# Kernel optimization log

Hardware: AMD Instinct MI355X
Metric: run time of the kernel (lower is better)

## Reference

```python
import jax, jax.numpy as jnp
import numpy as np


def lstm_cell(x, h, c, Wi, Wh, b):
    # PyTorch LSTMCell gate order: i, f, g, o
    g = x @ Wi.T + h @ Wh.T + b
    i, f, gg, o = jnp.split(g, 4, axis=-1)
    c = jax.nn.sigmoid(f) * c + jax.nn.sigmoid(i) * jnp.tanh(gg)
    h = jax.nn.sigmoid(o) * jnp.tanh(c)
    return h, c


def setup_inputs() -> dict:
    key = jax.random.key(0)
    ks = jax.random.split(key, 32)
    S, B, L, N, T = 20, 16, 30, 6, 20
    H, E, Vs, Vt = 512, 512, 50000, 30000
    w = lambda k, shape: jax.random.normal(k, shape, jnp.float32) * 0.05
    return {
        'articles': jax.random.randint(ks[0], (S, B, L), 0, Vs, jnp.int32),
        'summaries': jax.random.randint(ks[1], (N, B, T), 0, Vt, jnp.int32),
        'emb_src': w(ks[2], (Vs, E)),
        'emb_tgt': w(ks[3], (Vt, E)),
        'we_Wi': w(ks[4], (4 * H, E)), 'we_Wh': w(ks[5], (4 * H, H)), 'we_b': w(ks[6], (4 * H,)),
        'se_Wi': w(ks[7], (4 * H, H)), 'se_Wh': w(ks[8], (4 * H, H)), 'se_b': w(ks[9], (4 * H,)),
        'W_feat': w(ks[10], (H, H)), 'b_feat': w(ks[11], (H,)),
        'wd_Wi': w(ks[12], (4 * H, E)), 'wd_Wh': w(ks[13], (4 * H, H)), 'wd_b': w(ks[14], (4 * H,)),
        'W_vocab': w(ks[15], (Vt, H)), 'b_vocab': w(ks[16], (Vt,)),
        'sd_Wi': w(ks[17], (4 * H, H)), 'sd_Wh': w(ks[18], (4 * H, H)), 'sd_b': w(ks[19], (4 * H,)),
        'attn_Wh': w(ks[20], (H, H)), 'attn_wc': w(ks[21], (H,)), 'attn_v': w(ks[22], (H,)),
        'W_out': w(ks[23], (H, 2 * H)), 'b_out': w(ks[24], (H,)),
    }


def _forward(articles, summaries, emb_src, emb_tgt, we_Wi, we_Wh, we_b,
             se_Wi, se_Wh, se_b, W_feat, b_feat, wd_Wi, wd_Wh, wd_b,
             W_vocab, b_vocab, sd_Wi, sd_Wh, sd_b, attn_Wh, attn_wc, attn_v,
             W_out, b_out):
    S, B, L = articles.shape
    H = we_Wh.shape[1]

    # ---- word encoder: LSTMCell over each sentence, vmapped over S ----
    def encode_sentence(tokens):  # [B, L]
        x = emb_src[tokens]  # [B, L, E]
        z = jnp.zeros((B, H), x.dtype)
        def step(hc, xt):
            h, c = lstm_cell(xt, hc[0], hc[1], we_Wi, we_Wh, we_b)
            return (h, c), None
        (h, _), _ = jax.lax.scan(step, (z, z), jnp.swapaxes(x, 0, 1))
        return h
    word_hx = jax.vmap(encode_sentence)(articles)  # [S, B, H]

    # ---- sentence encoder: LSTM over sentence dim ----
    z = jnp.zeros((B, H), word_hx.dtype)
    def senc_step(hc, x):
        h, c = lstm_cell(x, hc[0], hc[1], se_Wi, se_Wh, se_b)
        return (h, c), h
    (s_hx, s_cx), sent_out = jax.lax.scan(senc_step, (z, z), word_hx)  # sent_out [S,B,H]
    sent_feat = sent_out @ W_feat.T + b_feat  # precomputed attention features

    mask = (articles[:, :, 0:1] > 0).astype(jnp.float32)  # [S, B, 1]
    coverage0 = jnp.zeros_like(mask)

    # ---- hierarchical decoder over summary sentences ----
    def sent_step(carry, sent):  # sent [B, T]
        w_hx, w_cx, s_hx, s_cx, coverage, loss = carry
        seq = sent.T  # [T, B]

        def word_step(wc, ba):
            wh, wcell, l = wc
            wb, wa = ba
            wh, wcell = lstm_cell(emb_tgt[wb], wh, wcell, wd_Wi, wd_Wh, wd_b)
            logits = wh @ W_vocab.T + b_vocab  # [B, V]
            logp = jax.nn.log_softmax(logits, axis=-1)
            nll = -jnp.take_along_axis(logp, wa[:, None], axis=1)[:, 0]
            m = (wa != 0).astype(logits.dtype)  # ignore_index=0
            l = l + jnp.sum(nll * m) / jnp.maximum(jnp.sum(m), 1.0)
            return (wh, wcell, l), None

        (w_hx, w_cx, loss), _ = jax.lax.scan(word_step, (w_hx, w_cx, loss), (seq[:-1], seq[1:]))

        # sentence decoder step with coverage attention over S sentences
        s_h2, s_cx = lstm_cell(w_hx, s_hx, s_cx, sd_Wi, sd_Wh, sd_b)
        e = jnp.einsum('sbh,h->sb', jnp.tanh(sent_feat + s_h2 @ attn_Wh.T + coverage * attn_wc), attn_v)
        e = jnp.where(mask[:, :, 0] > 0, e, -1e9)
        align = jax.nn.softmax(e, axis=0)[:, :, None]  # [S, B, 1]
        context = jnp.sum(align * sent_out, axis=0)  # [B, H]
        final = jnp.tanh(jnp.concatenate([context, s_h2], axis=-1) @ W_out.T + b_out)
        # coverage loss (with pre-update coverage), then accumulate coverage
        loss = loss + jnp.mean(jnp.sum(jnp.minimum(align[:, :, 0], coverage[:, :, 0]), axis=0))
        coverage = coverage + align
        return (final, w_cx, final, s_cx, coverage, loss), None

    init = (s_hx, s_cx, s_hx, s_cx, coverage0, jnp.float32(0.0))
    (_, _, _, _, _, loss), _ = jax.lax.scan(sent_step, init, summaries)
    return loss


def reference(articles, summaries, emb_src, emb_tgt, we_Wi, we_Wh, we_b,
              se_Wi, se_Wh, se_b, W_feat, b_feat, wd_Wi, wd_Wh, wd_b,
              W_vocab, b_vocab, sd_Wi, sd_Wh, sd_b, attn_Wh, attn_wc, attn_v,
              W_out, b_out):
    return _forward(articles, summaries, emb_src, emb_tgt, we_Wi, we_Wh, we_b,
                    se_Wi, se_Wh, se_b, W_feat, b_feat, wd_Wi, wd_Wh, wd_b,
                    W_vocab, b_vocab, sd_Wi, sd_Wh, sd_b, attn_Wh, attn_wc,
                    attn_v, W_out, b_out)
```

## Files before the change

### kernel.cpp

```cpp
#include <hip/hip_runtime.h>
#include <cstdint>
#include <cstddef>

#define H 512
#define SS 20
#define BB 16
#define LL 30
#define NN 6
#define TT 20
#define VT 30000
#define MROWS 1824
#define NSTEPS 114
#define MPAD 1856
#define NT2 120
#define UBLK 16
#define NV 232
#define MEGA 248

#define SCOPE_AGENT __HIP_MEMORY_SCOPE_AGENT

typedef __attribute__((ext_vector_type(8))) short bf16x8;
typedef __attribute__((ext_vector_type(4))) float f32x4;

__device__ __forceinline__ float sigmoidf_(float x) { return 1.f / (1.f + expf(-x)); }
__device__ __forceinline__ float b2f(ushort u) { return __uint_as_float(((uint32_t)u) << 16); }
__device__ __forceinline__ ushort f2b_rne(float f) {
  uint32_t u = __float_as_uint(f);
  return (ushort)((u + 0x7fffu + ((u >> 16) & 1u)) >> 16);
}

__device__ __forceinline__ void ast_u32(uint* p, uint v) {
  __hip_atomic_store(p, v, __ATOMIC_RELAXED, SCOPE_AGENT);
}
__device__ __forceinline__ uint ald_u32(const uint* p) {
  return __hip_atomic_load(p, __ATOMIC_RELAXED, SCOPE_AGENT);
}

__device__ __forceinline__ void sbar(uint* flags, int slot, int nblk, uint phase)
{
  __syncthreads();
  if (threadIdx.x == 0) {
    __builtin_amdgcn_fence(__ATOMIC_RELEASE, "agent");
    ast_u32(&flags[slot * 16], phase);
  }
  if ((int)threadIdx.x < nblk) {
    while (ald_u32(&flags[threadIdx.x * 16]) < phase)
      __builtin_amdgcn_s_sleep(1);
  }
  __syncthreads();
  if (threadIdx.x == 0)
    __builtin_amdgcn_fence(__ATOMIC_ACQUIRE, "agent");
  __syncthreads();
}

struct PrepP {
  const int* articles; const int* summaries;
  const float* emb_src; const float* emb_tgt;
  const float* we_Wi; const float* wd_Wi; const float* we_Wh;
  const float* se_Wi; const float* se_Wh; const float* W_feat;
  const float* wd_Wh; const float* sd_Wi; const float* sd_Wh;
  const float* attn_Wh; const float* W_out;
  ushort* A_we; ushort* A_wd;
  ushort* weWi; ushort* wdWi; ushort* weWh;
  ushort* seWi; ushort* seWh; ushort* wfeat;
  ushort* wdWh; ushort* sdWi; ushort* sdWh;
  ushort* attnWh; ushort* Wout;
};

__device__ __forceinline__ void conv_f2b(const float* __restrict__ src,
                                         ushort* __restrict__ dst, int n4,
                                         int t0, int stride)
{
  for (int i = t0; i < n4; i += stride) {
    float4 v = reinterpret_cast<const float4*>(src)[i];
    ushort4 o;
    o.x = f2b_rne(v.x); o.y = f2b_rne(v.y);
    o.z = f2b_rne(v.z); o.w = f2b_rne(v.w);
    reinterpret_cast<ushort4*>(dst)[i] = o;
  }
}

__global__ __launch_bounds__(256) void prep_kernel(PrepP P)
{
  const int t0 = blockIdx.x * 256 + threadIdx.x;
  const int stride = gridDim.x * 256;
  for (int i = t0; i < SS * BB * LL * H; i += stride) {
    int m = i >> 9, k = i & 511;
    int l = m / (SS * BB), sb = m % (SS * BB);
    int tok = P.articles[sb * LL + l];
    P.A_we[i] = f2b_rne(P.emb_src[(size_t)tok * H + k]);
  }
  for (int i = t0; i < MROWS * H; i += stride) {
    int m = i >> 9, k = i & 511;
    int stp = m >> 4, b = m & 15;
    int n = stp / (TT - 1), t = stp % (TT - 1);
    int tok = P.summaries[(n * BB + b) * TT + t];
    P.A_wd[i] = f2b_rne(P.emb_tgt[(size_t)tok * H + k]);
  }
  const int Q = 4 * H * H / 4;
  conv_f2b(P.we_Wi, P.weWi, Q, t0, stride);
  conv_f2b(P.wd_Wi, P.wdWi, Q, t0, stride);
  conv_f2b(P.we_Wh, P.weWh, Q, t0, stride);
  conv_f2b(P.se_Wi, P.seWi, Q, t0, stride);
  conv_f2b(P.se_Wh, P.seWh, Q, t0, stride);
  conv_f2b(P.wd_Wh, P.wdWh, Q, t0, stride);
  conv_f2b(P.sd_Wi, P.sdWi, Q, t0, stride);
  conv_f2b(P.sd_Wh, P.sdWh, Q, t0, stride);
  conv_f2b(P.W_feat, P.wfeat, H * H / 4, t0, stride);
  conv_f2b(P.attn_Wh, P.attnWh, H * H / 4, t0, stride);
  conv_f2b(P.W_out, P.Wout, H * 2 * H / 4, t0, stride);
}

__global__ __launch_bounds__(512) void proj_mfma_kernel(
    const ushort* __restrict__ A_we, const ushort* __restrict__ weWi,
    const float* __restrict__ we_b, ushort* __restrict__ XiW,
    const ushort* __restrict__ A_wd, const ushort* __restrict__ wdWi,
    const float* __restrict__ wd_b, ushort* __restrict__ XiD)
{
  int bid = blockIdx.x;
  const ushort* A; const ushort* W; const float* bias; ushort* C; int M, mt, nt;
  if (bid < 1200) { A = A_we; W = weWi; bias = we_b; C = XiW; M = 9600; mt = bid >> 3; nt = bid & 7; }
  else { int b2 = bid - 1200; A = A_wd; W = wdWi; bias = wd_b; C = XiD; M = MROWS; mt = b2 >> 3; nt = b2 & 7; }
  const int tid = threadIdx.x, wid = tid >> 6, lane = tid & 63;
  const int wm = wid >> 2, wn = wid & 3;
  const int m0 = mt * 64 + wm * 32, n0 = nt * 256 + wn * 64;
  const int lr = lane & 15, lk = (lane >> 4) << 3;

  f32x4 acc[2][4];
#pragma unroll
  for (int i = 0; i < 2; ++i)
#pragma unroll
    for (int nf = 0; nf < 4; ++nf) acc[i][nf] = (f32x4)0.0f;

  for (int k0 = 0; k0 < H; k0 += 32) {
    bf16x8 a[2], b[4];
#pragma unroll
    for (int i = 0; i < 2; ++i) {
      int m = m0 + i * 16 + lr;
      bf16x8 az = (bf16x8)(short)0;
      if (m < M) az = *reinterpret_cast<const bf16x8*>(A + (size_t)m * H + k0 + lk);
      a[i] = az;
    }
#pragma unroll
    for (int nf = 0; nf < 4; ++nf)
      b[nf] = *reinterpret_cast<const bf16x8*>(W + (size_t)(n0 + nf * 16 + lr) * H + k0 + lk);
#pragma unroll
    for (int i = 0; i < 2; ++i)
#pragma unroll
      for (int nf = 0; nf < 4; ++nf)
        acc[i][nf] = __builtin_amdgcn_mfma_f32_16x16x32_bf16(a[i], b[nf], acc[i][nf], 0, 0, 0);
  }
#pragma unroll
  for (int i = 0; i < 2; ++i)
#pragma unroll
    for (int nf = 0; nf < 4; ++nf) {
      int n = n0 + nf * 16 + lr;
      float bv = bias[n];
#pragma unroll
      for (int jreg = 0; jreg < 4; ++jreg) {
        int row = m0 + i * 16 + (lane >> 4) * 4 + jreg;
        if (row < M) C[(size_t)row * 2048 + n] = f2b_rne(acc[i][nf][jreg] + bv);
      }
    }
}

struct MP {
  const ushort* XiW; const ushort* XiD;
  const ushort* weWh; const ushort* seWi; const ushort* seWh;
  const ushort* wfeat; const ushort* wdWh; const ushort* sdWi;
  const ushort* sdWh; const ushort* attnWh; const ushort* Wout;
  const float* se_b; const float* b_feat; const float* sd_b; const float* b_out;
  const float* attn_wc; const float* attn_v; const int* articles;
  ushort* h0; ushort* h1;
  float* XiS;
  ushort* sh0; ushort* sh1;
  float* sent_out; ushort* sent_out_bf; float* sent_feat;
  ushort* wh_bf; ushort* sdh_bf; ushort* final_bf; ushort* catb;
  float* qb; float* ebuf; float* alignb; float* covb; float* loss;
  uint* sflags;
  uint* vbflags;
  uint* vflag;
  const float* Wv; ushort* Wv_bf; const float* bv; float* partials;
};

__global__ __launch_bounds__(512) void mega_kernel(MP P)
{
  const int tid = threadIdx.x, bid = blockIdx.x;
  const int wid = tid >> 6, lane = tid & 63;
  const int lr = lane & 15;
  const int lk = (lane >> 4) << 3;
  const int orow = (lane >> 4) << 2;

  if (bid >= UBLK) {
    const int v = bid - UBLK;
    const int mt = v >> 3, chunk = v & 7;
    __shared__ float red[4][64][2];

    if (tid == 0) {
      while (ald_u32(P.vflag) < 1u) __builtin_amdgcn_s_sleep(16);
    }
    __syncthreads();
    {
      const int n4 = VT * H / 4;
      for (int i = v * 512 + tid; i < n4; i += NV * 512) {
        float4 w = reinterpret_cast<const float4*>(P.Wv)[i];
        ushort4 o;
        o.x = f2b_rne(w.x); o.y = f2b_rne(w.y);
        o.z = f2b_rne(w.z); o.w = f2b_rne(w.w);
        reinterpret_cast<ushort4*>(P.Wv_bf)[i] = o;
      }
    }
    sbar(P.vbflags, v, NV, 1u);

    {
      int lastStep = mt * 4 + 3; if (lastStep > 113) lastStep = 113;
      uint want = 2u + (uint)(lastStep / 19);
      if (tid == 0) {
        while (ald_u32(P.vflag) < want) __builtin_amdgcn_s_sleep(16);
        __builtin_amdgcn_fence(__ATOMIC_ACQUIRE, "agent");
      }
      __syncthreads();
    }

    const int wm = wid >> 2, wn = wid & 3;
    const int m0 = mt * 64 + wm * 32;
    bf16x8 areg[2][16];
#pragma unroll
    for (int i = 0; i < 2; ++i)
#pragma unroll
      for (int kk = 0; kk < 16; ++kk)
        areg[i][kk] = *reinterpret_cast<const bf16x8*>(
            P.wh_bf + (size_t)(m0 + i * 16 + lr) * H + kk * 32 + lk);

    for (int nt2 = 0; nt2 < 15; ++nt2) {
      const int n0 = chunk * 3840 + nt2 * 256 + wn * 64;
      f32x4 acc[2][4];
#pragma unroll
      for (int i = 0; i < 2; ++i)
#pragma unroll
        for (int nf = 0; nf < 4; ++nf) acc[i][nf] = (f32x4)0.0f;

#pragma unroll 4
      for (int kk = 0; kk < 16; ++kk) {
        bf16x8 b[4];
#pragma unroll
        for (int nf = 0; nf < 4; ++nf) {
          int n = n0 + nf * 16 + lr;
          bf16x8 bz = (bf16x8)(short)0;
          if (n < VT) bz = *reinterpret_cast<const bf16x8*>(P.Wv_bf + (size_t)n * H + kk * 32 + lk);
          b[nf] = bz;
        }
#pragma unroll
        for (int i = 0; i < 2; ++i)
#pragma unroll
          for (int nf = 0; nf < 4; ++nf)
            acc[i][nf] = __builtin_amdgcn_mfma_f32_16x16x32_bf16(areg[i][kk], b[nf], acc[i][nf], 0, 0, 0);
      }

      float bc[4];
      int val[4];
#pragma unroll
      for (int nf = 0; nf < 4; ++nf) {
        int n = n0 + nf * 16 + lr;
        val[nf] = (n < VT);
        bc[nf] = val[nf] ? P.bv[n] : 0.f;
      }
#pragma unroll
      for (int i = 0; i < 2; ++i) {
#pragma unroll
        for (int jreg = 0; jreg < 4; ++jreg) {
          float lg[4];
          float mx = -3.0e38f;
#pragma unroll
          for (int nf = 0; nf < 4; ++nf) {
            lg[nf] = val[nf] ? (acc[i][nf][jreg] + bc[nf]) : -3.0e38f;
            mx = fmaxf(mx, lg[nf]);
          }
#pragma unroll
          for (int d = 1; d < 16; d <<= 1) mx = fmaxf(mx, __shfl_xor(mx, d));
          float s = 0.f;
#pragma unroll
          for (int nf = 0; nf < 4; ++nf) s += val[nf] ? expf(lg[nf] - mx) : 0.f;
#pragma unroll
          for (int d = 1; d < 16; d <<= 1) s += __shfl_xor(s, d);
          if (lr == 0) {
            int rloc = wm * 32 + i * 16 + (lane >> 4) * 4 + jreg;
            red[wn][rloc][0] = mx;
            red[wn][rloc][1] = s;
          }
        }
      }
      __syncthreads();
      if (tid < 64) {
        int r2 = tid;
        float M = -3.0e38f;
#pragma unroll
        for (int w = 0; w < 4; ++w) M = fmaxf(M, red[w][r2][0]);
        float S = 0.f;
#pragma unroll
        for (int w = 0; w < 4; ++w) S += red[w][r2][1] * expf(red[w][r2][0] - M);
        size_t p = ((size_t)(mt * 64 + r2) * NT2 + chunk * 15 + nt2) * 2;
        P.partials[p] = M;
        P.partials[p + 1] = S;
      }
      __syncthreads();
    }
    return;
  }

  __shared__ f32x4 hred[2][4][64];
  const int gw = bid * 8 + wid;
  uint ph = 0;

  {
    float cst[5][4];
#pragma unroll
    for (int it = 0; it < 5; ++it)
#pragma unroll
      for (int rg = 0; rg < 4; ++rg) cst[it][rg] = 0.f;
    ushort* cur = P.h0;
    ushort* nxt = P.h1;
    const int ug = gw & 31;
    const int unit = ug * 16 + lr;
    const ushort* wb = P.weWh + (size_t)(ug * 16 + lr) * H + lk;
    for (int l = 0; l < LL; ++l) {
#pragma unroll
      for (int it = 0; it < 5; ++it) {
        int mt = (gw + it * 128) >> 5;
        f32x4 acc[4];
#pragma unroll
        for (int g = 0; g < 4; ++g) acc[g] = (f32x4)0.0f;
        const ushort* ab = cur + (size_t)(mt * 16 + lr) * H + lk;
#pragma unroll
        for (int k0 = 0; k0 < H; k0 += 32) {
          bf16x8 a = *reinterpret_cast<const bf16x8*>(ab + k0);
#pragma unroll
          for (int g = 0; g < 4; ++g) {
            bf16x8 b = *reinterpret_cast<const bf16x8*>(wb + (size_t)g * H * H + k0);
            acc[g] = __builtin_amdgcn_mfma_f32_16x16x32_bf16(a, b, acc[g], 0, 0, 0);
          }
        }
#pragma unroll
        for (int rg = 0; rg < 4; ++rg) {
          int row = mt * 16 + orow + rg;
          const ushort* xi = P.XiW + (size_t)(l * 320 + row) * 2048 + unit;
          float gi = acc[0][rg] + b2f(xi[0]);
          float gf = acc[1][rg] + b2f(xi[512]);
          float gc = acc[2][rg] + b2f(xi[1024]);
          float go = acc[3][rg] + b2f(xi[1536]);
          float c = sigmoidf_(gf) * cst[it][rg] + sigmoidf_(gi) * tanhf(gc);
          float h = sigmoidf_(go) * tanhf(c);
          cst[it][rg] = c;
          nxt[(size_t)row * H + unit] = f2b_rne(h);
        }
      }
      sbar(P.sflags, bid, UBLK, ++ph);
      ushort* t = cur; cur = nxt; nxt = t;
    }
    {
      const ushort* wbs = P.seWi + (size_t)(ug * 16 + lr) * H + lk;
#pragma unroll
      for (int it = 0; it < 5; ++it) {
        int mt = (gw + it * 128) >> 5;
        f32x4 acc[4];
#pragma unroll
        for (int g = 0; g < 4; ++g) acc[g] = (f32x4)0.0f;
        const ushort* ab = cur + (size_t)(mt * 16 + lr) * H + lk;
#pragma unroll
        for (int k0 = 0; k0 < H; k0 += 32) {
          bf16x8 a = *reinterpret_cast<const bf16x8*>(ab + k0);
#pragma unroll
          for (int g = 0; g < 4; ++g) {
            bf16x8 b = *reinterpret_cast<const bf16x8*>(wbs + (size_t)g * H * H + k0);
            acc[g] = __builtin_amdgcn_mfma_f32_16x16x32_bf16(a, b, acc[g], 0, 0, 0);
          }
        }
#pragma unroll
        for (int rg = 0; rg < 4; ++rg) {
          int row = mt * 16 + orow + rg;
#pragma unroll
          for (int g = 0; g < 4; ++g)
            P.XiS[(size_t)row * 2048 + g * H + unit] = acc[g][rg] + P.se_b[g * H + unit];
        }
      }
    }
    sbar(P.sflags, bid, UBLK, ++ph);
    if (bid == 0 && tid == 0)
      __hip_atomic_store(P.vflag, 1u, __ATOMIC_RELEASE, SCOPE_AGENT);
  }

  float cw[4] = {0.f, 0.f, 0.f, 0.f};
  float csd[4] = {0.f, 0.f, 0.f, 0.f};
  {
    float cse[4] = {0.f, 0.f, 0.f, 0.f};
    ushort* cur = P.sh0;
    ushort* nxt = P.sh1;
    const int ug = bid * 2 + wid;
    const int unit = ug * 16 + lr;
    for (int s = 0; s < SS; ++s) {
      if (wid < 2) {
        f32x4 acc[4];
#pragma unroll
        for (int g = 0; g < 4; ++g) acc[g] = (f32x4)0.0f;
        const ushort* ab = cur + (size_t)lr * H + lk;
        const ushort* wb = P.seWh + (size_t)(ug * 16 + lr) * H + lk;
#pragma unroll
        for (int k0 = 0; k0 < H; k0 += 32) {
          bf16x8 a = *reinterpret_cast<const bf16x8*>(ab + k0);
#pragma unroll
          for (int g = 0; g < 4; ++g) {
            bf16x8 b = *reinterpret_cast<const bf16x8*>(wb + (size_t)g * H * H + k0);
            acc[g] = __builtin_amdgcn_mfma_f32_16x16x32_bf16(a, b, acc[g], 0, 0, 0);
          }
        }
#pragma unroll
        for (int rg = 0; rg < 4; ++rg) {
          int row = orow + rg;
          const float* xi = P.XiS + (size_t)(s * 16 + row) * 2048 + unit;
          float gi = acc[0][rg] + xi[0];
          float gf = acc[1][rg] + xi[512];
          float gc = acc[2][rg] + xi[1024];
          float go = acc[3][rg] + xi[1536];
          float c = sigmoidf_(gf) * cse[rg] + sigmoidf_(gi) * tanhf(gc);
          float h = sigmoidf_(go) * tanhf(c);
          cse[rg] = c;
          nxt[(size_t)row * H + unit] = f2b_rne(h);
          P.sent_out[(size_t)(s * 16 + row) * H + unit] = h;
          P.sent_out_bf[(size_t)(s * 16 + row) * H + unit] = f2b_rne(h);
        }
      }
      sbar(P.sflags, bid, UBLK, ++ph);
      ushort* t = cur; cur = nxt; nxt = t;
    }
    if (wid < 2) {
      f32x4 v; v[0] = cse[0]; v[1] = cse[1]; v[2] = cse[2]; v[3] = cse[3];
      hred[wid][0][lane] = v;
#pragma unroll
      for (int rg = 0; rg < 4; ++rg) csd[rg] = cse[rg];
    }
    __syncthreads();
    if (wid < 4 && !(wid & 1)) {
      f32x4 v = hred[wid >> 1][0][lane];
      cw[0] = v[0]; cw[1] = v[1]; cw[2] = v[2]; cw[3] = v[3];
    }
    __syncthreads();
  }

  {
    const int ug = gw & 31;
    const int unit = ug * 16 + lr;
    const ushort* wb = P.wfeat + (size_t)(ug * 16 + lr) * H + lk;
#pragma unroll
    for (int it = 0; it < 5; ++it) {
      int mt = (gw + it * 128) >> 5;
      f32x4 acc = (f32x4)0.0f;
      const ushort* ab = P.sent_out_bf + (size_t)(mt * 16 + lr) * H + lk;
#pragma unroll
      for (int k0 = 0; k0 < H; k0 += 32) {
        bf16x8 a = *reinterpret_cast<const bf16x8*>(ab + k0);
        bf16x8 b = *reinterpret_cast<const bf16x8*>(wb + k0);
        acc = __builtin_amdgcn_mfma_f32_16x16x32_bf16(a, b, acc, 0, 0, 0);
      }
#pragma unroll
      for (int rg = 0; rg < 4; ++rg) {
        int row = mt * 16 + orow + rg;
        P.sent_feat[(size_t)row * H + unit] = acc[rg] + P.b_feat[unit];
      }
    }
    sbar(P.sflags, bid, UBLK, ++ph);
  }

  {
    const int half = wid & 1;
    const int ug2 = bid * 2 + (wid >> 1);
    const int unit2 = ug2 * 16 + lr;
    const int ug = bid * 2 + wid;
    const int unit = ug * 16 + lr;

    for (int n = 0; n < NN; ++n) {
      bf16x8 wreg[4][8];
      if (wid < 4) {
#pragma unroll
        for (int g = 0; g < 4; ++g)
#pragma unroll
          for (int kk = 0; kk < 8; ++kk)
            wreg[g][kk] = *reinterpret_cast<const bf16x8*>(
                P.wdWh + (size_t)g * H * H + (size_t)(ug2 * 16 + lr) * H +
                half * 256 + kk * 32 + lk);
      }
      for (int t = 0; t < TT - 1; ++t) {
        int stp = n * (TT - 1) + t;
        f32x4 acc[4];
        if (wid < 4) {
          const ushort* A = (t == 0)
              ? ((n == 0) ? P.sh0 : P.final_bf)
              : P.wh_bf + (size_t)(stp - 1) * 16 * H;
#pragma unroll
          for (int g = 0; g < 4; ++g) acc[g] = (f32x4)0.0f;
          const ushort* ab = A + (size_t)lr * H + half * 256 + lk;
#pragma unroll
          for (int kk = 0; kk < 8; ++kk) {
            bf16x8 a = *reinterpret_cast<const bf16x8*>(ab + kk * 32);
#pragma unroll
            for (int g = 0; g < 4; ++g)
              acc[g] = __builtin_amdgcn_mfma_f32_16x16x32_bf16(a, wreg[g][kk], acc[g], 0, 0, 0);
          }
          if (half) {
#pragma unroll
            for (int g = 0; g < 4; ++g) hred[wid >> 1][g][lane] = acc[g];
          }
        }
        __syncthreads();
        if (wid < 4 && !half) {
#pragma unroll
          for (int g = 0; g < 4; ++g) acc[g] += hred[wid >> 1][g][lane];
#pragma unroll
          for (int rg = 0; rg < 4; ++rg) {
            int row = orow + rg;
            const ushort* xi = P.XiD + (size_t)(stp * 16 + row) * 2048 + unit2;
            float gi = acc[0][rg] + b2f(xi[0]);
            float gf = acc[1][rg] + b2f(xi[512]);
            float gc = acc[2][rg] + b2f(xi[1024]);
            float go = acc[3][rg] + b2f(xi[1536]);
            float c = sigmoidf_(gf) * cw[rg] + sigmoidf_(gi) * tanhf(gc);
            float h = sigmoidf_(go) * tanhf(c);
            cw[rg] = c;
            P.wh_bf[(size_t)(stp * 16 + row) * H + unit2] = f2b_rne(h);
          }
        }
        sbar(P.sflags, bid, UBLK, ++ph);
      }
      if (bid == 0 && tid == 0)
        __hip_atomic_store(P.vflag, 2u + (uint)n, __ATOMIC_RELEASE, SCOPE_AGENT);
      if (wid < 2) {
        f32x4 acc[4];
#pragma unroll
        for (int g = 0; g < 4; ++g) acc[g] = (f32x4)0.0f;
        const ushort* A1 = P.wh_bf + (size_t)(n * (TT - 1) + TT - 2) * 16 * H;
        const ushort* A2 = (n == 0) ? P.sh0 : P.final_bf;
        const ushort* ab1 = A1 + (size_t)lr * H + lk;
        const ushort* wb1 = P.sdWi + (size_t)(ug * 16 + lr) * H + lk;
#pragma unroll
        for (int k0 = 0; k0 < H; k0 += 32) {
          bf16x8 a = *reinterpret_cast<const bf16x8*>(ab1 + k0);
#pragma unroll
          for (int g = 0; g < 4; ++g) {
            bf16x8 b = *reinterpret_cast<const bf16x8*>(wb1 + (size_t)g * H * H + k0);
            acc[g] = __builtin_amdgcn_mfma_f32_16x16x32_bf16(a, b, acc[g], 0, 0, 0);
          }
        }
        const ushort* ab2 = A2 + (size_t)lr * H + lk;
        const ushort* wb2 = P.sdWh + (size_t)(ug * 16 + lr) * H + lk;
#pragma unroll
        for (int k0 = 0; k0 < H; k0 += 32) {
          bf16x8 a = *reinterpret_cast<const bf16x8*>(ab2 + k0);
#pragma unroll
          for (int g = 0; g < 4; ++g) {
            bf16x8 b = *reinterpret_cast<const bf16x8*>(wb2 + (size_t)g * H * H + k0);
            acc[g] = __builtin_amdgcn_mfma_f32_16x16x32_bf16(a, b, acc[g], 0, 0, 0);
          }
        }
#pragma unroll
        for (int rg = 0; rg < 4; ++rg) {
          int row = orow + rg;
          float gi = acc[0][rg] + P.sd_b[0 * H + unit];
          float gf = acc[1][rg] + P.sd_b[1 * H + unit];
          float gc = acc[2][rg] + P.sd_b[2 * H + unit];
          float go = acc[3][rg] + P.sd_b[3 * H + unit];
          float c = sigmoidf_(gf) * csd[rg] + sigmoidf_(gi) * tanhf(gc);
          float h = sigmoidf_(go) * tanhf(c);
          csd[rg] = c;
          P.sdh_bf[(size_t)row * H + unit] = f2b_rne(h);
        }
      }
      sbar(P.sflags, bid, UBLK, ++ph);
      if (wid < 2) {
        f32x4 acc = (f32x4)0.0f;
        const ushort* ab = P.sdh_bf + (size_t)lr * H + lk;
        const ushort* wb = P.attnWh + (size_t)(ug * 16 + lr) * H + lk;
#pragma unroll
        for (int k0 = 0; k0 < H; k0 += 32) {
          bf16x8 a = *reinterpret_cast<const bf16x8*>(ab + k0);
          bf16x8 b = *reinterpret_cast<const bf16x8*>(wb + k0);
          acc = __builtin_amdgcn_mfma_f32_16x16x32_bf16(a, b, acc, 0, 0, 0);
        }
#pragma unroll
        for (int rg = 0; rg < 4; ++rg)
          P.qb[(size_t)(orow + rg) * H + unit] = acc[rg];
      }
      sbar(P.sflags, bid, UBLK, ++ph);
      for (int sb = gw; sb < 320; sb += 128) {
        int b = sb & 15;
        float cov = P.covb[sb];
        float sum = 0.f;
        for (int h2 = lane; h2 < H; h2 += 64)
          sum += tanhf(P.sent_feat[(size_t)sb * H + h2] + P.qb[b * H + h2] +
                       cov * P.attn_wc[h2]) * P.attn_v[h2];
#pragma unroll
        for (int d = 1; d < 64; d <<= 1) sum += __shfl_xor(sum, d);
        if (lane == 0)
          P.ebuf[sb] = (P.articles[sb * LL] > 0) ? sum : -1e9f;
      }
      sbar(P.sflags, bid, UBLK, ++ph);
      if (wid == 0) {
        int b = bid;
        float ev = (lane < SS) ? P.ebuf[lane * 16 + b] : -3.0e38f;
        float mx = ev;
#pragma unroll
        for (int d = 1; d < 64; d <<= 1) mx = fmaxf(mx, __shfl_xor(mx, d));
        float ex = (lane < SS) ? expf(ev - mx) : 0.f;
        float s = ex;
#pragma unroll
        for (int d = 1; d < 64; d <<= 1) s += __shfl_xor(s, d);
        float al = ex / s;
        float cl = 0.f;
        if (lane < SS) {
          int sb = lane * 16 + b;
          float cov = P.covb[sb];
          cl = fminf(al, cov);
          P.covb[sb] = cov + al;
          P.alignb[sb] = al;
        }
#pragma unroll
        for (int d = 1; d < 64; d <<= 1) cl += __shfl_xor(cl, d);
        if (lane == 0) atomicAdd(P.loss, cl * (1.f / BB));
      }
      __syncthreads();
      {
        int b = bid, h2 = tid;
        float s = 0.f;
#pragma unroll
        for (int ss2 = 0; ss2 < SS; ++ss2)
          s += P.alignb[ss2 * 16 + b] * P.sent_out[(size_t)(ss2 * 16 + b) * H + h2];
        P.catb[b * 1024 + h2] = f2b_rne(s);
        P.catb[b * 1024 + 512 + h2] = P.sdh_bf[(size_t)b * H + h2];
      }
      sbar(P.sflags, bid, UBLK, ++ph);
      if (wid < 2) {
        f32x4 acc = (f32x4)0.0f;
        const ushort* ab = P.catb + (size_t)lr * 1024 + lk;
        const ushort* wb = P.Wout + (size_t)(ug * 16 + lr) * 1024 + lk;
#pragma unroll
        for (int k0 = 0; k0 < 1024; k0 += 32) {
          bf16x8 a = *reinterpret_cast<const bf16x8*>(ab + k0);
          bf16x8 b = *reinterpret_cast<const bf16x8*>(wb + k0);
          acc = __builtin_amdgcn_mfma_f32_16x16x32_bf16(a, b, acc, 0, 0, 0);
        }
#pragma unroll
        for (int rg = 0; rg < 4; ++rg) {
          int row = orow + rg;
          float v = tanhf(acc[rg] + P.b_out[unit]);
          P.final_bf[(size_t)row * H + unit] = f2b_rne(v);
        }
      }
      sbar(P.sflags, bid, UBLK, ++ph);
    }
    if (bid == 0 && tid == 0)
      __hip_atomic_store(P.vflag, 7u, __ATOMIC_RELEASE, SCOPE_AGENT);
  }
}

__global__ void tlog_kernel(const ushort* __restrict__ wh_bf,
                            const ushort* __restrict__ Wv_bf,
                            const float* __restrict__ bv,
                            const int* __restrict__ summaries,
                            float* __restrict__ tlog)
{
  int row = blockIdx.x;
  int lane = threadIdx.x;
  int b = row & 15, stp = row >> 4;
  int n = stp / (TT - 1), t = stp % (TT - 1);
  int tgt = summaries[(n * BB + b) * TT + t + 1];
  float s = 0.f;
  for (int k = lane; k < H; k += 64)
    s += b2f(wh_bf[(size_t)row * H + k]) * b2f(Wv_bf[(size_t)tgt * H + k]);
#pragma unroll
  for (int d = 1; d < 64; d <<= 1) s += __shfl_xor(s, d);
  if (lane == 0) tlog[row] = s + bv[tgt];
}

__global__ __launch_bounds__(256) void nll_kernel(
    const float* __restrict__ partials, const float* __restrict__ tlog,
    const int* __restrict__ summaries, float* __restrict__ loss)
{
  int stp = blockIdx.x;
  int tid = threadIdx.x;
  int rr = tid >> 4, ch = tid & 15;
  int row = stp * 16 + rr;
  const float* pr = partials + (size_t)row * NT2 * 2;
  float mx = -3.0e38f;
  for (int t2 = ch; t2 < NT2; t2 += 16) mx = fmaxf(mx, pr[t2 * 2]);
#pragma unroll
  for (int d = 1; d < 16; d <<= 1) mx = fmaxf(mx, __shfl_xor(mx, d));
  float s = 0.f;
  for (int t2 = ch; t2 < NT2; t2 += 16) s += pr[t2 * 2 + 1] * expf(pr[t2 * 2] - mx);
#pragma unroll
  for (int d = 1; d < 16; d <<= 1) s += __shfl_xor(s, d);
  __shared__ float sh_n[16], sh_m[16];
  if (ch == 0) {
    float lse = mx + logf(s);
    float nll = lse - tlog[row];
    int b = row & 15;
    int n = stp / (TT - 1), t = stp % (TT - 1);
    int wa = summaries[(n * BB + b) * TT + t + 1];
    sh_n[rr] = (wa != 0) ? nll : 0.f;
    sh_m[rr] = (wa != 0) ? 1.f : 0.f;
  }
  __syncthreads();
  if (tid == 0) {
    float sn = 0.f, sm = 0.f;
    for (int r2 = 0; r2 < 16; ++r2) { sn += sh_n[r2]; sm += sh_m[r2]; }
    atomicAdd(loss, sn / fmaxf(sm, 1.f));
  }
}

extern "C" void kernel_launch(void* const* d_in, const int* in_sizes, int n_in,
                              void* d_out, int out_size, void* d_ws, size_t ws_size,
                              hipStream_t stream)
{
  (void)in_sizes; (void)n_in; (void)out_size; (void)ws_size;
  const int*   articles  = (const int*)d_in[0];
  const int*   summaries = (const int*)d_in[1];
  const float* emb_src   = (const float*)d_in[2];
  const float* emb_tgt   = (const float*)d_in[3];
  const float* we_Wi = (const float*)d_in[4];
  const float* we_Wh = (const float*)d_in[5];
  const float* we_b  = (const float*)d_in[6];
  const float* se_Wi = (const float*)d_in[7];
  const float* se_Wh = (const float*)d_in[8];
  const float* se_b  = (const float*)d_in[9];
  const float* W_feat = (const float*)d_in[10];
  const float* b_feat = (const float*)d_in[11];
  const float* wd_Wi = (const float*)d_in[12];
  const float* wd_Wh = (const float*)d_in[13];
  const float* wd_b  = (const float*)d_in[14];
  const float* W_vocab = (const float*)d_in[15];
  const float* b_vocab = (const float*)d_in[16];
  const float* sd_Wi = (const float*)d_in[17];
  const float* sd_Wh = (const float*)d_in[18];
  const float* sd_b  = (const float*)d_in[19];
  const float* attn_Wh = (const float*)d_in[20];
  const float* attn_wc = (const float*)d_in[21];
  const float* attn_v  = (const float*)d_in[22];
  const float* W_out = (const float*)d_in[23];
  const float* b_out = (const float*)d_in[24];

  char* wsb = (char*)d_ws;
  size_t off = 0;
  auto alloc = [&](size_t bytes) -> char* {
    char* p = wsb + off;
    off += (bytes + 255) & ~(size_t)255;
    return p;
  };

  char* regA = alloc(9830400);
  ushort* A_we     = (ushort*)regA;
  ushort* wh_bf    = (ushort*)regA;
  float*  partials = (float*)(regA + 1900544);
  float*  tlogb    = (float*)(regA + 3682304);

  ushort* A_wd = (ushort*)alloc((size_t)MROWS * H * 2);

  char* regW = alloc((size_t)9600 * 2048 * 2);
  ushort* XiW   = (ushort*)regW;
  ushort* Wv_bf = (ushort*)regW;

  ushort* XiD = (ushort*)alloc((size_t)MROWS * 2048 * 2);

  ushort* weWi  = (ushort*)alloc(4 * H * H * 2);
  ushort* wdWi  = (ushort*)alloc(4 * H * H * 2);
  ushort* weWh  = (ushort*)alloc(4 * H * H * 2);
  ushort* seWi  = (ushort*)alloc(4 * H * H * 2);
  ushort* seWh  = (ushort*)alloc(4 * H * H * 2);
  ushort* wdWh  = (ushort*)alloc(4 * H * H * 2);
  ushort* sdWi  = (ushort*)alloc(4 * H * H * 2);
  ushort* sdWh  = (ushort*)alloc(4 * H * H * 2);
  ushort* wfeat = (ushort*)alloc(H * H * 2);
  ushort* attnWh= (ushort*)alloc(H * H * 2);
  ushort* Wout  = (ushort*)alloc(H * 2 * H * 2);

  float*  XiS = (float*)alloc((size_t)320 * 2048 * 4);
  ushort* h0  = (ushort*)alloc(320 * H * 2);
  ushort* h1  = (ushort*)alloc(320 * H * 2);
  ushort* sh0 = (ushort*)alloc(16 * H * 2);
  ushort* sh1 = (ushort*)alloc(16 * H * 2);
  float*  sent_out    = (float*)alloc(320 * H * 4);
  ushort* sent_out_bf = (ushort*)alloc(320 * H * 2);
  float*  sent_feat   = (float*)alloc(320 * H * 4);
  ushort* sdh_bf   = (ushort*)alloc(16 * H * 2);
  ushort* final_bf = (ushort*)alloc(16 * H * 2);
  ushort* catb     = (ushort*)alloc(16 * 1024 * 2);
  float*  qb       = (float*)alloc(16 * H * 4);
  float*  ebuf   = (float*)alloc(1280);
  float*  alignb = (float*)alloc(1280);
  float*  covb   = (float*)alloc(1280);
  uint*   sflags  = (uint*)alloc(UBLK * 16 * 4);
  uint*   vbflags = (uint*)alloc(NV * 16 * 4);
  uint*   vflag   = (uint*)alloc(256);

  float* loss = (float*)d_out;
  hipMemsetAsync(loss, 0, 4, stream);
  hipMemsetAsync(covb, 0, 1280, stream);
  hipMemsetAsync(h0, 0, 320 * H * 2, stream);
  hipMemsetAsync(sh0, 0, 16 * H * 2, stream);
  hipMemsetAsync(sflags, 0, UBLK * 16 * 4, stream);
  hipMemsetAsync(vbflags, 0, NV * 16 * 4, stream);
  hipMemsetAsync(vflag, 0, 256, stream);

  {
    PrepP P = {articles, summaries, emb_src, emb_tgt,
               we_Wi, wd_Wi, we_Wh, se_Wi, se_Wh, W_feat,
               wd_Wh, sd_Wi, sd_Wh, attn_Wh, W_out,
               A_we, A_wd, weWi, wdWi, weWh, seWi, seWh, wfeat,
               wdWh, sdWi, sdWh, attnWh, Wout};
    prep_kernel<<<2048, 256, 0, stream>>>(P);
  }

  proj_mfma_kernel<<<1432, 512, 0, stream>>>(A_we, weWi, we_b, XiW,
                                             A_wd, wdWi, wd_b, XiD);

  hipMemsetAsync((char*)wh_bf + (size_t)MROWS * H * 2, 0,
                 (size_t)(MPAD - MROWS) * H * 2, stream);

  {
    MP P;
    P.XiW = XiW; P.XiD = XiD;
    P.weWh = weWh; P.seWi = seWi; P.seWh = seWh; P.wfeat = wfeat;
    P.wdWh = wdWh; P.sdWi = sdWi; P.sdWh = sdWh; P.attnWh = attnWh; P.Wout = Wout;
    P.se_b = se_b; P.b_feat = b_feat; P.sd_b = sd_b; P.b_out = b_out;
    P.attn_wc = attn_wc; P.attn_v = attn_v; P.articles = articles;
    P.h0 = h0; P.h1 = h1; P.XiS = XiS; P.sh0 = sh0; P.sh1 = sh1;
    P.sent_out = sent_out; P.sent_out_bf = sent_out_bf; P.sent_feat = sent_feat;
    P.wh_bf = wh_bf; P.sdh_bf = sdh_bf; P.final_bf = final_bf; P.catb = catb;
    P.qb = qb; P.ebuf = ebuf; P.alignb = alignb; P.covb = covb; P.loss = loss;
    P.sflags = sflags; P.vbflags = vbflags; P.vflag = vflag;
    P.Wv = W_vocab; P.Wv_bf = Wv_bf; P.bv = b_vocab; P.partials = partials;
    mega_kernel<<<MEGA, 512, 0, stream>>>(P);
  }

  tlog_kernel<<<MROWS, 64, 0, stream>>>(wh_bf, Wv_bf, b_vocab, summaries, tlogb);
  nll_kernel<<<NSTEPS, 256, 0, stream>>>(partials, tlogb, summaries, loss);
}
```

Measured before the change: 5.032 ms.

## Partition recurrent LSTM work per batch element to eliminate grid-wide barriers

```diff
diff --git a/kernel.cpp b/kernel.cpp
--- a/kernel.cpp
+++ b/kernel.cpp
@@ -28,7 +28,6 @@
   uint32_t u = __float_as_uint(f);
   return (ushort)((u + 0x7fffu + ((u >> 16) & 1u)) >> 16);
 }
-
 __device__ __forceinline__ void ast_u32(uint* p, uint v) {
   __hip_atomic_store(p, v, __ATOMIC_RELAXED, SCOPE_AGENT);
 }
@@ -164,6 +163,27 @@
     }
 }
 
+union SmemU {
+  struct {
+    ushort h[32 * 520];
+    float  c[20 * 512];
+  } we;
+  struct {
+    float  sf[20 * 512];
+    ushort so[20 * 520];
+    ushort senc_h[512];
+    ushort h[512];
+    ushort final_h[512];
+    ushort sdh[512];
+    ushort cat[1024];
+    float  qb[512];
+    float  e[20];
+    float  align[20];
+    float  cov[20];
+  } de;
+  struct { float red[4][64][2]; } vo;
+};
+
 struct MP {
   const ushort* XiW; const ushort* XiD;
   const ushort* weWh; const ushort* seWi; const ushort* seWh;
@@ -171,58 +191,88 @@
   const ushort* sdWh; const ushort* attnWh; const ushort* Wout;
   const float* se_b; const float* b_feat; const float* sd_b; const float* b_out;
   const float* attn_wc; const float* attn_v; const int* articles;
-  ushort* h0; ushort* h1;
   float* XiS;
-  ushort* sh0; ushort* sh1;
-  float* sent_out; ushort* sent_out_bf; float* sent_feat;
-  ushort* wh_bf; ushort* sdh_bf; ushort* final_bf; ushort* catb;
-  float* qb; float* ebuf; float* alignb; float* covb; float* loss;
-  uint* sflags;
+  ushort* wh_bf;
+  float* loss;
+  uint* prog;
   uint* vbflags;
-  uint* vflag;
   const float* Wv; ushort* Wv_bf; const float* bv; float* partials;
 };
 
+__device__ __forceinline__ void mm1g(const ushort* hsrc, const ushort* W,
+                                     int w, int lr, int lk, f32x4 acc[4][4])
+{
+#pragma unroll 4
+  for (int kt = 0; kt < 16; ++kt) {
+    int k0 = kt * 32;
+    bf16x8 a = *reinterpret_cast<const bf16x8*>(hsrc + k0 + lk);
+#pragma unroll
+    for (int g = 0; g < 4; ++g)
+#pragma unroll
+      for (int nf = 0; nf < 4; ++nf) {
+        int col = g * 512 + w * 64 + nf * 16 + lr;
+        bf16x8 b = *reinterpret_cast<const bf16x8*>(W + (size_t)col * H + k0 + lk);
+        acc[g][nf] = __builtin_amdgcn_mfma_f32_16x16x32_bf16(a, b, acc[g][nf], 0, 0, 0);
+      }
+  }
+}
+
+__device__ __forceinline__ void mm1p(const ushort* hsrc, const ushort* W, int K,
+                                     int w, int lr, int lk, f32x4 acc4[4])
+{
+  for (int k0 = 0; k0 < K; k0 += 32) {
+    bf16x8 a = *reinterpret_cast<const bf16x8*>(hsrc + k0 + lk);
+#pragma unroll
+    for (int nf = 0; nf < 4; ++nf) {
+      int col = w * 64 + nf * 16 + lr;
+      bf16x8 b = *reinterpret_cast<const bf16x8*>(W + (size_t)col * K + k0 + lk);
+      acc4[nf] = __builtin_amdgcn_mfma_f32_16x16x32_bf16(a, b, acc4[nf], 0, 0, 0);
+    }
+  }
+}
+
 __global__ __launch_bounds__(512) void mega_kernel(MP P)
 {
+  __shared__ SmemU sm;
   const int tid = threadIdx.x, bid = blockIdx.x;
-  const int wid = tid >> 6, lane = tid & 63;
+  const int w = tid >> 6, lane = tid & 63;
   const int lr = lane & 15;
   const int lk = (lane >> 4) << 3;
-  const int orow = (lane >> 4) << 2;
+  const bool row0 = (lane >> 4) == 0;
 
   if (bid >= UBLK) {
     const int v = bid - UBLK;
     const int mt = v >> 3, chunk = v & 7;
-    __shared__ float red[4][64][2];
 
     if (tid == 0) {
-      while (ald_u32(P.vflag) < 1u) __builtin_amdgcn_s_sleep(16);
+      for (int b = 0; b < UBLK; ++b)
+        while (ald_u32(&P.prog[b * 16]) < 1u) __builtin_amdgcn_s_sleep(16);
     }
     __syncthreads();
     {
       const int n4 = VT * H / 4;
       for (int i = v * 512 + tid; i < n4; i += NV * 512) {
-        float4 w = reinterpret_cast<const float4*>(P.Wv)[i];
+        float4 x = reinterpret_cast<const float4*>(P.Wv)[i];
         ushort4 o;
-        o.x = f2b_rne(w.x); o.y = f2b_rne(w.y);
-        o.z = f2b_rne(w.z); o.w = f2b_rne(w.w);
+        o.x = f2b_rne(x.x); o.y = f2b_rne(x.y);
+        o.z = f2b_rne(x.z); o.w = f2b_rne(x.w);
         reinterpret_cast<ushort4*>(P.Wv_bf)[i] = o;
       }
     }
     sbar(P.vbflags, v, NV, 1u);
 
     {
-      int lastStep = mt * 4 + 3; if (lastStep > 113) lastStep = 113;
-      uint want = 2u + (uint)(lastStep / 19);
+      int lastStep = mt * 4 + 3; if (lastStep > NSTEPS - 1) lastStep = NSTEPS - 1;
+      uint want = 2u + (uint)(lastStep / (TT - 1));
       if (tid == 0) {
-        while (ald_u32(P.vflag) < want) __builtin_amdgcn_s_sleep(16);
+        for (int b = 0; b < UBLK; ++b)
+          while (ald_u32(&P.prog[b * 16]) < want) __builtin_amdgcn_s_sleep(16);
         __builtin_amdgcn_fence(__ATOMIC_ACQUIRE, "agent");
       }
       __syncthreads();
     }
 
-    const int wm = wid >> 2, wn = wid & 3;
+    const int wm = w >> 2, wn = w & 3;
     const int m0 = mt * 64 + wm * 32;
     bf16x8 areg[2][16];
 #pragma unroll
@@ -239,7 +289,6 @@
       for (int i = 0; i < 2; ++i)
 #pragma unroll
         for (int nf = 0; nf < 4; ++nf) acc[i][nf] = (f32x4)0.0f;
-
 #pragma unroll 4
       for (int kk = 0; kk < 16; ++kk) {
         bf16x8 b[4];
@@ -256,9 +305,7 @@
           for (int nf = 0; nf < 4; ++nf)
             acc[i][nf] = __builtin_amdgcn_mfma_f32_16x16x32_bf16(areg[i][kk], b[nf], acc[i][nf], 0, 0, 0);
       }
-
-      float bc[4];
-      int val[4];
+      float bc[4]; int val[4];
 #pragma unroll
       for (int nf = 0; nf < 4; ++nf) {
         int n = n0 + nf * 16 + lr;
@@ -269,8 +316,7 @@
       for (int i = 0; i < 2; ++i) {
 #pragma unroll
         for (int jreg = 0; jreg < 4; ++jreg) {
-          float lg[4];
-          float mx = -3.0e38f;
+          float lg[4], mx = -3.0e38f;
 #pragma unroll
           for (int nf = 0; nf < 4; ++nf) {
             lg[nf] = val[nf] ? (acc[i][nf][jreg] + bc[nf]) : -3.0e38f;
@@ -285,21 +331,20 @@
           for (int d = 1; d < 16; d <<= 1) s += __shfl_xor(s, d);
           if (lr == 0) {
             int rloc = wm * 32 + i * 16 + (lane >> 4) * 4 + jreg;
-            red[wn][rloc][0] = mx;
-            red[wn][rloc][1] = s;
+            sm.vo.red[wn][rloc][0] = mx;
+            sm.vo.red[wn][rloc][1] = s;
           }
         }
       }
       __syncthreads();
       if (tid < 64) {
-        int r2 = tid;
         float M = -3.0e38f;
 #pragma unroll
-        for (int w = 0; w < 4; ++w) M = fmaxf(M, red[w][r2][0]);
+        for (int q = 0; q < 4; ++q) M = fmaxf(M, sm.vo.red[q][tid][0]);
         float S = 0.f;
 #pragma unroll
-        for (int w = 0; w < 4; ++w) S += red[w][r2][1] * expf(red[w][r2][0] - M);
-        size_t p = ((size_t)(mt * 64 + r2) * NT2 + chunk * 15 + nt2) * 2;
+        for (int q = 0; q < 4; ++q) S += sm.vo.red[q][tid][1] * expf(sm.vo.red[q][tid][0] - M);
+        size_t p = ((size_t)(mt * 64 + tid) * NT2 + chunk * 15 + nt2) * 2;
         P.partials[p] = M;
         P.partials[p + 1] = S;
       }
@@ -308,355 +353,325 @@
     return;
   }
 
-  __shared__ f32x4 hred[2][4][64];
-  const int gw = bid * 8 + wid;
-  uint ph = 0;
+  const int b_ = bid;
 
   {
-    float cst[5][4];
-#pragma unroll
-    for (int it = 0; it < 5; ++it)
-#pragma unroll
-      for (int rg = 0; rg < 4; ++rg) cst[it][rg] = 0.f;
-    ushort* cur = P.h0;
-    ushort* nxt = P.h1;
-    const int ug = gw & 31;
-    const int unit = ug * 16 + lr;
-    const ushort* wb = P.weWh + (size_t)(ug * 16 + lr) * H + lk;
+    for (int i = tid; i < 32 * 520; i += 512) sm.we.h[i] = 0;
+    for (int i = tid; i < 20 * 512; i += 512) sm.we.c[i] = 0.f;
+    __syncthreads();
+
     for (int l = 0; l < LL; ++l) {
-#pragma unroll
-      for (int it = 0; it < 5; ++it) {
-        int mt = (gw + it * 128) >> 5;
-        f32x4 acc[4];
-#pragma unroll
-        for (int g = 0; g < 4; ++g) acc[g] = (f32x4)0.0f;
-        const ushort* ab = cur + (size_t)(mt * 16 + lr) * H + lk;
-#pragma unroll
-        for (int k0 = 0; k0 < H; k0 += 32) {
-          bf16x8 a = *reinterpret_cast<const bf16x8*>(ab + k0);
-#pragma unroll
-          for (int g = 0; g < 4; ++g) {
-            bf16x8 b = *reinterpret_cast<const bf16x8*>(wb + (size_t)g * H * H + k0);
-            acc[g] = __builtin_amdgcn_mfma_f32_16x16x32_bf16(a, b, acc[g], 0, 0, 0);
+      f32x4 acc[4][2][4];
+#pragma unroll
+      for (int g = 0; g < 4; ++g)
+#pragma unroll
+        for (int mt = 0; mt < 2; ++mt)
+#pragma unroll
+          for (int nf = 0; nf < 4; ++nf) acc[g][mt][nf] = (f32x4)0.0f;
+#pragma unroll 2
+      for (int kt = 0; kt < 16; ++kt) {
+        int k0 = kt * 32;
+        bf16x8 a[2];
+#pragma unroll
+        for (int mt = 0; mt < 2; ++mt)
+          a[mt] = *reinterpret_cast<const bf16x8*>(&sm.we.h[(mt * 16 + lr) * 520 + k0 + lk]);
+#pragma unroll
+        for (int g = 0; g < 4; ++g)
+#pragma unroll
+          for (int nf = 0; nf < 4; ++nf) {
+            int col = g * 512 + w * 64 + nf * 16 + lr;
+            bf16x8 bb = *reinterpret_cast<const bf16x8*>(P.weWh + (size_t)col * H + k0 + lk);
+#pragma unroll
+            for (int mt = 0; mt < 2; ++mt)
+              acc[g][mt][nf] = __builtin_amdgcn_mfma_f32_16x16x32_bf16(a[mt], bb, acc[g][mt][nf], 0, 0, 0);
+          }
+      }
+      __syncthreads();
+#pragma unroll
+      for (int mt = 0; mt < 2; ++mt)
+#pragma unroll
+        for (int reg = 0; reg < 4; ++reg) {
+          int s = mt * 16 + (lane >> 4) * 4 + reg;
+          if (s < SS) {
+#pragma unroll
+            for (int nf = 0; nf < 4; ++nf) {
+              int u = w * 64 + nf * 16 + lr;
+              const ushort* xi = P.XiW + (size_t)(l * 320 + s * 16 + b_) * 2048 + u;
+              float gi = acc[0][mt][nf][reg] + b2f(xi[0]);
+              float gf = acc[1][mt][nf][reg] + b2f(xi[512]);
+              float gc = acc[2][mt][nf][reg] + b2f(xi[1024]);
+              float go = acc[3][mt][nf][reg] + b2f(xi[1536]);
+              float c = sigmoidf_(gf) * sm.we.c[s * 512 + u] + sigmoidf_(gi) * tanhf(gc);
+              float h = sigmoidf_(go) * tanhf(c);
+              sm.we.c[s * 512 + u] = c;
+              sm.we.h[s * 520 + u] = f2b_rne(h);
+            }
           }
         }
-#pragma unroll
-        for (int rg = 0; rg < 4; ++rg) {
-          int row = mt * 16 + orow + rg;
-          const ushort* xi = P.XiW + (size_t)(l * 320 + row) * 2048 + unit;
-          float gi = acc[0][rg] + b2f(xi[0]);
-          float gf = acc[1][rg] + b2f(xi[512]);
-          float gc = acc[2][rg] + b2f(xi[1024]);
-          float go = acc[3][rg] + b2f(xi[1536]);
-          float c = sigmoidf_(gf) * cst[it][rg] + sigmoidf_(gi) * tanhf(gc);
-          float h = sigmoidf_(go) * tanhf(c);
-          cst[it][rg] = c;
-          nxt[(size_t)row * H + unit] = f2b_rne(h);
-        }
-      }
-      sbar(P.sflags, bid, UBLK, ++ph);
-      ushort* t = cur; cur = nxt; nxt = t;
-    }
+      __syncthreads();
+    }
+
     {
-      const ushort* wbs = P.seWi + (size_t)(ug * 16 + lr) * H + lk;
-#pragma unroll
-      for (int it = 0; it < 5; ++it) {
-        int mt = (gw + it * 128) >> 5;
-        f32x4 acc[4];
-#pragma unroll
-        for (int g = 0; g < 4; ++g) acc[g] = (f32x4)0.0f;
-        const ushort* ab = cur + (size_t)(mt * 16 + lr) * H + lk;
-#pragma unroll
-        for (int k0 = 0; k0 < H; k0 += 32) {
-          bf16x8 a = *reinterpret_cast<const bf16x8*>(ab + k0);
-#pragma unroll
-          for (int g = 0; g < 4; ++g) {
-            bf16x8 b = *reinterpret_cast<const bf16x8*>(wbs + (size_t)g * H * H + k0);
-            acc[g] = __builtin_amdgcn_mfma_f32_16x16x32_bf16(a, b, acc[g], 0, 0, 0);
+      f32x4 acc[4][2][4];
+#pragma unroll
+      for (int g = 0; g < 4; ++g)
+#pragma unroll
+        for (int mt = 0; mt < 2; ++mt)
+#pragma unroll
+          for (int nf = 0; nf < 4; ++nf) acc[g][mt][nf] = (f32x4)0.0f;
+#pragma unroll 2
+      for (int kt = 0; kt < 16; ++kt) {
+        int k0 = kt * 32;
+        bf16x8 a[2];
+#pragma unroll
+        for (int mt = 0; mt < 2; ++mt)
+          a[mt] = *reinterpret_cast<const bf16x8*>(&sm.we.h[(mt * 16 + lr) * 520 + k0 + lk]);
+#pragma unroll
+        for (int g = 0; g < 4; ++g)
+#pragma unroll
+          for (int nf = 0; nf < 4; ++nf) {
+            int col = g * 512 + w * 64 + nf * 16 + lr;
+            bf16x8 bb = *reinterpret_cast<const bf16x8*>(P.seWi + (size_t)col * H + k0 + lk);
+#pragma unroll
+            for (int mt = 0; mt < 2; ++mt)
+              acc[g][mt][nf] = __builtin_amdgcn_mfma_f32_16x16x32_bf16(a[mt], bb, acc[g][mt][nf], 0, 0, 0);
+          }
+      }
+#pragma unroll
+      for (int mt = 0; mt < 2; ++mt)
+#pragma unroll
+        for (int reg = 0; reg < 4; ++reg) {
+          int s = mt * 16 + (lane >> 4) * 4 + reg;
+          if (s < SS) {
+#pragma unroll
+            for (int nf = 0; nf < 4; ++nf) {
+              int u = w * 64 + nf * 16 + lr;
+#pragma unroll
+              for (int g = 0; g < 4; ++g)
+                P.XiS[(size_t)(s * 16 + b_) * 2048 + g * 512 + u] =
+                    acc[g][mt][nf][reg] + P.se_b[g * 512 + u];
+            }
           }
         }
-#pragma unroll
-        for (int rg = 0; rg < 4; ++rg) {
-          int row = mt * 16 + orow + rg;
-#pragma unroll
-          for (int g = 0; g < 4; ++g)
-            P.XiS[(size_t)row * 2048 + g * H + unit] = acc[g][rg] + P.se_b[g * H + unit];
+    }
+    __syncthreads();
+    if (tid == 0) {
+      __builtin_amdgcn_fence(__ATOMIC_RELEASE, "agent");
+      ast_u32(&P.prog[b_ * 16], 1u);
+    }
+  }
+
+  float cse[4] = {0.f, 0.f, 0.f, 0.f};
+  {
+    for (int i = tid; i < 512; i += 512) sm.de.senc_h[i] = 0;
+    __syncthreads();
+    for (int s = 0; s < SS; ++s) {
+      f32x4 acc[4][4];
+#pragma unroll
+      for (int g = 0; g < 4; ++g)
+#pragma unroll
+        for (int nf = 0; nf < 4; ++nf) acc[g][nf] = (f32x4)0.0f;
+      mm1g(sm.de.senc_h, P.seWh, w, lr, lk, acc);
+      __syncthreads();
+      if (row0) {
+#pragma unroll
+        for (int nf = 0; nf < 4; ++nf) {
+          int u = w * 64 + nf * 16 + lr;
+          const float* xi = P.XiS + (size_t)(s * 16 + b_) * 2048 + u;
+          float gi = acc[0][nf][0] + xi[0];
+          float gf = acc[1][nf][0] + xi[512];
+          float gc = acc[2][nf][0] + xi[1024];
+          float go = acc[3][nf][0] + xi[1536];
+          float c = sigmoidf_(gf) * cse[nf] + sigmoidf_(gi) * tanhf(gc);
+          float h = sigmoidf_(go) * tanhf(c);
+          cse[nf] = c;
+          ushort hb = f2b_rne(h);
+          sm.de.senc_h[u] = hb;
+          sm.de.so[s * 520 + u] = hb;
         }
       }
-    }
-    sbar(P.sflags, bid, UBLK, ++ph);
-    if (bid == 0 && tid == 0)
-      __hip_atomic_store(P.vflag, 1u, __ATOMIC_RELEASE, SCOPE_AGENT);
-  }
-
-  float cw[4] = {0.f, 0.f, 0.f, 0.f};
-  float csd[4] = {0.f, 0.f, 0.f, 0.f};
+      __syncthreads();
+    }
+  }
+
   {
-    float cse[4] = {0.f, 0.f, 0.f, 0.f};
-    ushort* cur = P.sh0;
-    ushort* nxt = P.sh1;
-    const int ug = bid * 2 + wid;
-    const int unit = ug * 16 + lr;
-    for (int s = 0; s < SS; ++s) {
-      if (wid < 2) {
-        f32x4 acc[4];
-#pragma unroll
-        for (int g = 0; g < 4; ++g) acc[g] = (f32x4)0.0f;
-        const ushort* ab = cur + (size_t)lr * H + lk;
-        const ushort* wb = P.seWh + (size_t)(ug * 16 + lr) * H + lk;
-#pragma unroll
-        for (int k0 = 0; k0 < H; k0 += 32) {
-          bf16x8 a = *reinterpret_cast<const bf16x8*>(ab + k0);
-#pragma unroll
-          for (int g = 0; g < 4; ++g) {
-            bf16x8 b = *reinterpret_cast<const bf16x8*>(wb + (size_t)g * H * H + k0);
-            acc[g] = __builtin_amdgcn_mfma_f32_16x16x32_bf16(a, b, acc[g], 0, 0, 0);
+    f32x4 acc2[2][4];
+#pragma unroll
+    for (int mt = 0; mt < 2; ++mt)
+#pragma unroll
+      for (int nf = 0; nf < 4; ++nf) acc2[mt][nf] = (f32x4)0.0f;
+#pragma unroll 2
+    for (int kt = 0; kt < 16; ++kt) {
+      int k0 = kt * 32;
+      bf16x8 a[2];
+#pragma unroll
+      for (int mt = 0; mt < 2; ++mt)
+        a[mt] = *reinterpret_cast<const bf16x8*>(&sm.de.so[(mt * 16 + lr) * 520 + k0 + lk]);
+#pragma unroll
+      for (int nf = 0; nf < 4; ++nf) {
+        int col = w * 64 + nf * 16 + lr;
+        bf16x8 bb = *reinterpret_cast<const bf16x8*>(P.wfeat + (size_t)col * H + k0 + lk);
+#pragma unroll
+        for (int mt = 0; mt < 2; ++mt)
+          acc2[mt][nf] = __builtin_amdgcn_mfma_f32_16x16x32_bf16(a[mt], bb, acc2[mt][nf], 0, 0, 0);
+      }
+    }
+    __syncthreads();
+#pragma unroll
+    for (int mt = 0; mt < 2; ++mt)
+#pragma unroll
+      for (int reg = 0; reg < 4; ++reg) {
+        int s = mt * 16 + (lane >> 4) * 4 + reg;
+        if (s < SS) {
+#pragma unroll
+          for (int nf = 0; nf < 4; ++nf) {
+            int u = w * 64 + nf * 16 + lr;
+            sm.de.sf[s * 512 + u] = acc2[mt][nf][reg] + P.b_feat[u];
           }
         }
-#pragma unroll
-        for (int rg = 0; rg < 4; ++rg) {
-          int row = orow + rg;
-          const float* xi = P.XiS + (size_t)(s * 16 + row) * 2048 + unit;
-          float gi = acc[0][rg] + xi[0];
-          float gf = acc[1][rg] + xi[512];
-          float gc = acc[2][rg] + xi[1024];
-          float go = acc[3][rg] + xi[1536];
-          float c = sigmoidf_(gf) * cse[rg] + sigmoidf_(gi) * tanhf(gc);
+      }
+    if (tid < SS) sm.de.cov[tid] = 0.f;
+    __syncthreads();
+  }
+
+  float cw[4], csd[4];
+#pragma unroll
+  for (int nf = 0; nf < 4; ++nf) { cw[nf] = cse[nf]; csd[nf] = cse[nf]; }
+
+  for (int n = 0; n < NN; ++n) {
+    {
+      const ushort* src = (n == 0) ? sm.de.senc_h : sm.de.final_h;
+      if (tid < 512) sm.de.h[tid] = src[tid];
+      __syncthreads();
+    }
+    for (int t = 0; t < TT - 1; ++t) {
+      int stp = n * (TT - 1) + t;
+      f32x4 acc[4][4];
+#pragma unroll
+      for (int g = 0; g < 4; ++g)
+#pragma unroll
+        for (int nf = 0; nf < 4; ++nf) acc[g][nf] = (f32x4)0.0f;
+      mm1g(sm.de.h, P.wdWh, w, lr, lk, acc);
+      __syncthreads();
+      if (row0) {
+#pragma unroll
+        for (int nf = 0; nf < 4; ++nf) {
+          int u = w * 64 + nf * 16 + lr;
+          const ushort* xi = P.XiD + (size_t)(stp * 16 + b_) * 2048 + u;
+          float gi = acc[0][nf][0] + b2f(xi[0]);
+          float gf = acc[1][nf][0] + b2f(xi[512]);
+          float gc = acc[2][nf][0] + b2f(xi[1024]);
+          float go = acc[3][nf][0] + b2f(xi[1536]);
+          float c = sigmoidf_(gf) * cw[nf] + sigmoidf_(gi) * tanhf(gc);
           float h = sigmoidf_(go) * tanhf(c);
-          cse[rg] = c;
-          nxt[(size_t)row * H + unit] = f2b_rne(h);
-          P.sent_out[(size_t)(s * 16 + row) * H + unit] = h;
-          P.sent_out_bf[(size_t)(s * 16 + row) * H + unit] = f2b_rne(h);
+          cw[nf] = c;
+          ushort hb = f2b_rne(h);
+          sm.de.h[u] = hb;
+          P.wh_bf[(size_t)(stp * 16 + b_) * H + u] = hb;
         }
       }
-      sbar(P.sflags, bid, UBLK, ++ph);
-      ushort* t = cur; cur = nxt; nxt = t;
-    }
-    if (wid < 2) {
-      f32x4 v; v[0] = cse[0]; v[1] = cse[1]; v[2] = cse[2]; v[3] = cse[3];
-      hred[wid][0][lane] = v;
-#pragma unroll
-      for (int rg = 0; rg < 4; ++rg) csd[rg] = cse[rg];
+      __syncthreads();
+    }
+    if (tid == 0) {
+      __builtin_amdgcn_fence(__ATOMIC_RELEASE, "agent");
+      ast_u32(&P.prog[b_ * 16], 2u + (uint)n);
+    }
+    {
+      f32x4 acc[4][4];
+#pragma unroll
+      for (int g = 0; g < 4; ++g)
+#pragma unroll
+        for (int nf = 0; nf < 4; ++nf) acc[g][nf] = (f32x4)0.0f;
+      mm1g(sm.de.h, P.sdWi, w, lr, lk, acc);
+      mm1g((n == 0) ? sm.de.senc_h : sm.de.final_h, P.sdWh, w, lr, lk, acc);
+      __syncthreads();
+      if (row0) {
+#pragma unroll
+        for (int nf = 0; nf < 4; ++nf) {
+          int u = w * 64 + nf * 16 + lr;
+          float gi = acc[0][nf][0] + P.sd_b[0 * 512 + u];
+          float gf = acc[1][nf][0] + P.sd_b[1 * 512 + u];
+          float gc = acc[2][nf][0] + P.sd_b[2 * 512 + u];
+          float go = acc[3][nf][0] + P.sd_b[3 * 512 + u];
+          float c = sigmoidf_(gf) * csd[nf] + sigmoidf_(gi) * tanhf(gc);
+          float h = sigmoidf_(go) * tanhf(c);
+          csd[nf] = c;
+          sm.de.sdh[u] = f2b_rne(h);
+        }
+      }
+      __syncthreads();
+    }
+    {
+      f32x4 a4[4];
+#pragma unroll
+      for (int nf = 0; nf < 4; ++nf) a4[nf] = (f32x4)0.0f;
+      mm1p(sm.de.sdh, P.attnWh, H, w, lr, lk, a4);
+      __syncthreads();
+      if (row0) {
+#pragma unroll
+        for (int nf = 0; nf < 4; ++nf)
+          sm.de.qb[w * 64 + nf * 16 + lr] = a4[nf][0];
+      }
+      __syncthreads();
+    }
+    for (int s = w; s < SS; s += 8) {
+      float cov = sm.de.cov[s];
+      float sum = 0.f;
+      for (int h2 = lane; h2 < H; h2 += 64)
+        sum += tanhf(sm.de.sf[s * 512 + h2] + sm.de.qb[h2] +
+                     cov * P.attn_wc[h2]) * P.attn_v[h2];
+#pragma unroll
+      for (int d = 1; d < 64; d <<= 1) sum += __shfl_xor(sum, d);
+      if (lane == 0)
+        sm.de.e[s] = (P.articles[(s * 16 + b_) * LL] > 0) ? sum : -1e9f;
     }
     __syncthreads();
-    if (wid < 4 && !(wid & 1)) {
-      f32x4 v = hred[wid >> 1][0][lane];
-      cw[0] = v[0]; cw[1] = v[1]; cw[2] = v[2]; cw[3] = v[3];
+    if (w == 0) {
+      float ev = (lane < SS) ? sm.de.e[lane] : -3.0e38f;
+      float mx = ev;
+#pragma unroll
+      for (int d = 1; d < 64; d <<= 1) mx = fmaxf(mx, __shfl_xor(mx, d));
+      float ex = (lane < SS) ? expf(ev - mx) : 0.f;
+      float s = ex;
+#pragma unroll
+      for (int d = 1; d < 64; d <<= 1) s += __shfl_xor(s, d);
+      float al = ex / s;
+      float cl = 0.f;
+      if (lane < SS) {
+        float cov = sm.de.cov[lane];
+        cl = fminf(al, cov);
+        sm.de.cov[lane] = cov + al;
+        sm.de.align[lane] = al;
+      }
+#pragma unroll
+      for (int d = 1; d < 64; d <<= 1) cl += __shfl_xor(cl, d);
+      if (lane == 0) atomicAdd(P.loss, cl * (1.f / BB));
     }
     __syncthreads();
-  }
-
-  {
-    const int ug = gw & 31;
-    const int unit = ug * 16 + lr;
-    const ushort* wb = P.wfeat + (size_t)(ug * 16 + lr) * H + lk;
-#pragma unroll
-    for (int it = 0; it < 5; ++it) {
-      int mt = (gw + it * 128) >> 5;
-      f32x4 acc = (f32x4)0.0f;
-      const ushort* ab = P.sent_out_bf + (size_t)(mt * 16 + lr) * H + lk;
-#pragma unroll
-      for (int k0 = 0; k0 < H; k0 += 32) {
-        bf16x8 a = *reinterpret_cast<const bf16x8*>(ab + k0);
-        bf16x8 b = *reinterpret_cast<const bf16x8*>(wb + k0);
-        acc = __builtin_amdgcn_mfma_f32_16x16x32_bf16(a, b, acc, 0, 0, 0);
-      }
-#pragma unroll
-      for (int rg = 0; rg < 4; ++rg) {
-        int row = mt * 16 + orow + rg;
-        P.sent_feat[(size_t)row * H + unit] = acc[rg] + P.b_feat[unit];
-      }
-    }
-    sbar(P.sflags, bid, UBLK, ++ph);
-  }
-
-  {
-    const int half = wid & 1;
-    const int ug2 = bid * 2 + (wid >> 1);
-    const int unit2 = ug2 * 16 + lr;
-    const int ug = bid * 2 + wid;
-    const int unit = ug * 16 + lr;
-
-    for (int n = 0; n < NN; ++n) {
-      bf16x8 wreg[4][8];
-      if (wid < 4) {
-#pragma unroll
-        for (int g = 0; g < 4; ++g)
-#pragma unroll
-          for (int kk = 0; kk < 8; ++kk)
-            wreg[g][kk] = *reinterpret_cast<const bf16x8*>(
-                P.wdWh + (size_t)g * H * H + (size_t)(ug2 * 16 + lr) * H +
-                half * 256 + kk * 32 + lk);
-      }
-      for (int t = 0; t < TT - 1; ++t) {
-        int stp = n * (TT - 1) + t;
-        f32x4 acc[4];
-        if (wid < 4) {
-          const ushort* A = (t == 0)
-              ? ((n == 0) ? P.sh0 : P.final_bf)
-              : P.wh_bf + (size_t)(stp - 1) * 16 * H;
-#pragma unroll
-          for (int g = 0; g < 4; ++g) acc[g] = (f32x4)0.0f;
-          const ushort* ab = A + (size_t)lr * H + half * 256 + lk;
-#pragma unroll
-          for (int kk = 0; kk < 8; ++kk) {
-            bf16x8 a = *reinterpret_cast<const bf16x8*>(ab + kk * 32);
-#pragma unroll
-            for (int g = 0; g < 4; ++g)
-              acc[g] = __builtin_amdgcn_mfma_f32_16x16x32_bf16(a, wreg[g][kk], acc[g], 0, 0, 0);
-          }
-          if (half) {
-#pragma unroll
-            for (int g = 0; g < 4; ++g) hred[wid >> 1][g][lane] = acc[g];
-          }
+    if (tid < 512) {
+      float s = 0.f;
+#pragma unroll
+      for (int ss2 = 0; ss2 < SS; ++ss2)
+        s += sm.de.align[ss2] * b2f(sm.de.so[ss2 * 520 + tid]);
+      sm.de.cat[tid] = f2b_rne(s);
+      sm.de.cat[512 + tid] = sm.de.sdh[tid];
+    }
+    __syncthreads();
+    {
+      f32x4 a4[4];
+#pragma unroll
+      for (int nf = 0; nf < 4; ++nf) a4[nf] = (f32x4)0.0f;
+      mm1p(sm.de.cat, P.Wout, 2 * H, w, lr, lk, a4);
+      __syncthreads();
+      if (row0) {
+#pragma unroll
+        for (int nf = 0; nf < 4; ++nf) {
+          int u = w * 64 + nf * 16 + lr;
+          sm.de.final_h[u] = f2b_rne(tanhf(a4[nf][0] + P.b_out[u]));
         }
-        __syncthreads();
-        if (wid < 4 && !half) {
-#pragma unroll
-          for (int g = 0; g < 4; ++g) acc[g] += hred[wid >> 1][g][lane];
-#pragma unroll
-          for (int rg = 0; rg < 4; ++rg) {
-            int row = orow + rg;
-            const ushort* xi = P.XiD + (size_t)(stp * 16 + row) * 2048 + unit2;
-            float gi = acc[0][rg] + b2f(xi[0]);
-            float gf = acc[1][rg] + b2f(xi[512]);
-            float gc = acc[2][rg] + b2f(xi[1024]);
-            float go = acc[3][rg] + b2f(xi[1536]);
-            float c = sigmoidf_(gf) * cw[rg] + sigmoidf_(gi) * tanhf(gc);
-            float h = sigmoidf_(go) * tanhf(c);
-            cw[rg] = c;
-            P.wh_bf[(size_t)(stp * 16 + row) * H + unit2] = f2b_rne(h);
-          }
-        }
-        sbar(P.sflags, bid, UBLK, ++ph);
-      }
-      if (bid == 0 && tid == 0)
-        __hip_atomic_store(P.vflag, 2u + (uint)n, __ATOMIC_RELEASE, SCOPE_AGENT);
-      if (wid < 2) {
-        f32x4 acc[4];
-#pragma unroll
-        for (int g = 0; g < 4; ++g) acc[g] = (f32x4)0.0f;
-        const ushort* A1 = P.wh_bf + (size_t)(n * (TT - 1) + TT - 2) * 16 * H;
-        const ushort* A2 = (n == 0) ? P.sh0 : P.final_bf;
-        const ushort* ab1 = A1 + (size_t)lr * H + lk;
-        const ushort* wb1 = P.sdWi + (size_t)(ug * 16 + lr) * H + lk;
-#pragma unroll
-        for (int k0 = 0; k0 < H; k0 += 32) {
-          bf16x8 a = *reinterpret_cast<const bf16x8*>(ab1 + k0);
-#pragma unroll
-          for (int g = 0; g < 4; ++g) {
-            bf16x8 b = *reinterpret_cast<const bf16x8*>(wb1 + (size_t)g * H * H + k0);
-            acc[g] = __builtin_amdgcn_mfma_f32_16x16x32_bf16(a, b, acc[g], 0, 0, 0);
-          }
-        }
-        const ushort* ab2 = A2 + (size_t)lr * H + lk;
-        const ushort* wb2 = P.sdWh + (size_t)(ug * 16 + lr) * H + lk;
-#pragma unroll
-        for (int k0 = 0; k0 < H; k0 += 32) {
-          bf16x8 a = *reinterpret_cast<const bf16x8*>(ab2 + k0);
-#pragma unroll
-          for (int g = 0; g < 4; ++g) {
-            bf16x8 b = *reinterpret_cast<const bf16x8*>(wb2 + (size_t)g * H * H + k0);
-            acc[g] = __builtin_amdgcn_mfma_f32_16x16x32_bf16(a, b, acc[g], 0, 0, 0);
-          }
-        }
-#pragma unroll
-        for (int rg = 0; rg < 4; ++rg) {
-          int row = orow + rg;
-          float gi = acc[0][rg] + P.sd_b[0 * H + unit];
-          float gf = acc[1][rg] + P.sd_b[1 * H + unit];
-          float gc = acc[2][rg] + P.sd_b[2 * H + unit];
-          float go = acc[3][rg] + P.sd_b[3 * H + unit];
-          float c = sigmoidf_(gf) * csd[rg] + sigmoidf_(gi) * tanhf(gc);
-          float h = sigmoidf_(go) * tanhf(c);
-          csd[rg] = c;
-          P.sdh_bf[(size_t)row * H + unit] = f2b_rne(h);
-        }
-      }
-      sbar(P.sflags, bid, UBLK, ++ph);
-      if (wid < 2) {
-        f32x4 acc = (f32x4)0.0f;
-        const ushort* ab = P.sdh_bf + (size_t)lr * H + lk;
-        const ushort* wb = P.attnWh + (size_t)(ug * 16 + lr) * H + lk;
-#pragma unroll
-        for (int k0 = 0; k0 < H; k0 += 32) {
-          bf16x8 a = *reinterpret_cast<const bf16x8*>(ab + k0);
-          bf16x8 b = *reinterpret_cast<const bf16x8*>(wb + k0);
-          acc = __builtin_amdgcn_mfma_f32_16x16x32_bf16(a, b, acc, 0, 0, 0);
-        }
-#pragma unroll
-        for (int rg = 0; rg < 4; ++rg)
-          P.qb[(size_t)(orow + rg) * H + unit] = acc[rg];
-      }
-      sbar(P.sflags, bid, UBLK, ++ph);
-      for (int sb = gw; sb < 320; sb += 128) {
-        int b = sb & 15;
-        float cov = P.covb[sb];
-        float sum = 0.f;
-        for (int h2 = lane; h2 < H; h2 += 64)
-          sum += tanhf(P.sent_feat[(size_t)sb * H + h2] + P.qb[b * H + h2] +
-                       cov * P.attn_wc[h2]) * P.attn_v[h2];
-#pragma unroll
-        for (int d = 1; d < 64; d <<= 1) sum += __shfl_xor(sum, d);
-        if (lane == 0)
-          P.ebuf[sb] = (P.articles[sb * LL] > 0) ? sum : -1e9f;
-      }
-      sbar(P.sflags, bid, UBLK, ++ph);
-      if (wid == 0) {
-        int b = bid;
-        float ev = (lane < SS) ? P.ebuf[lane * 16 + b] : -3.0e38f;
-        float mx = ev;
-#pragma unroll
-        for (int d = 1; d < 64; d <<= 1) mx = fmaxf(mx, __shfl_xor(mx, d));
-        float ex = (lane < SS) ? expf(ev - mx) : 0.f;
-        float s = ex;
-#pragma unroll
-        for (int d = 1; d < 64; d <<= 1) s += __shfl_xor(s, d);
-        float al = ex / s;
-        float cl = 0.f;
-        if (lane < SS) {
-          int sb = lane * 16 + b;
-          float cov = P.covb[sb];
-          cl = fminf(al, cov);
-          P.covb[sb] = cov + al;
-          P.alignb[sb] = al;
-        }
-#pragma unroll
-        for (int d = 1; d < 64; d <<= 1) cl += __shfl_xor(cl, d);
-        if (lane == 0) atomicAdd(P.loss, cl * (1.f / BB));
-      }
-      __syncthreads();
-      {
-        int b = bid, h2 = tid;
-        float s = 0.f;
-#pragma unroll
-        for (int ss2 = 0; ss2 < SS; ++ss2)
-          s += P.alignb[ss2 * 16 + b] * P.sent_out[(size_t)(ss2 * 16 + b) * H + h2];
-        P.catb[b * 1024 + h2] = f2b_rne(s);
-        P.catb[b * 1024 + 512 + h2] = P.sdh_bf[(size_t)b * H + h2];
-      }
-      sbar(P.sflags, bid, UBLK, ++ph);
-      if (wid < 2) {
-        f32x4 acc = (f32x4)0.0f;
-        const ushort* ab = P.catb + (size_t)lr * 1024 + lk;
-        const ushort* wb = P.Wout + (size_t)(ug * 16 + lr) * 1024 + lk;
-#pragma unroll
-        for (int k0 = 0; k0 < 1024; k0 += 32) {
-          bf16x8 a = *reinterpret_cast<const bf16x8*>(ab + k0);
-          bf16x8 b = *reinterpret_cast<const bf16x8*>(wb + k0);
-          acc = __builtin_amdgcn_mfma_f32_16x16x32_bf16(a, b, acc, 0, 0, 0);
-        }
-#pragma unroll
-        for (int rg = 0; rg < 4; ++rg) {
-          int row = orow + rg;
-          float v = tanhf(acc[rg] + P.b_out[unit]);
-          P.final_bf[(size_t)row * H + unit] = f2b_rne(v);
-        }
-      }
-      sbar(P.sflags, bid, UBLK, ++ph);
-    }
-    if (bid == 0 && tid == 0)
-      __hip_atomic_store(P.vflag, 7u, __ATOMIC_RELEASE, SCOPE_AGENT);
+      }
+      __syncthreads();
+    }
   }
 }
 
@@ -708,9 +723,9 @@
   }
   __syncthreads();
   if (tid == 0) {
-    float sn = 0.f, sm = 0.f;
-    for (int r2 = 0; r2 < 16; ++r2) { sn += sh_n[r2]; sm += sh_m[r2]; }
-    atomicAdd(loss, sn / fmaxf(sm, 1.f));
+    float sn = 0.f, smm = 0.f;
+    for (int r2 = 0; r2 < 16; ++r2) { sn += sh_n[r2]; smm += sh_m[r2]; }
+    atomicAdd(loss, sn / fmaxf(smm, 1.f));
   }
 }
 
@@ -779,33 +794,14 @@
   ushort* attnWh= (ushort*)alloc(H * H * 2);
   ushort* Wout  = (ushort*)alloc(H * 2 * H * 2);
 
-  float*  XiS = (float*)alloc((size_t)320 * 2048 * 4);
-  ushort* h0  = (ushort*)alloc(320 * H * 2);
-  ushort* h1  = (ushort*)alloc(320 * H * 2);
-  ushort* sh0 = (ushort*)alloc(16 * H * 2);
-  ushort* sh1 = (ushort*)alloc(16 * H * 2);
-  float*  sent_out    = (float*)alloc(320 * H * 4);
-  ushort* sent_out_bf = (ushort*)alloc(320 * H * 2);
-  float*  sent_feat   = (float*)alloc(320 * H * 4);
-  ushort* sdh_bf   = (ushort*)alloc(16 * H * 2);
-  ushort* final_bf = (ushort*)alloc(16 * H * 2);
-  ushort* catb     = (ushort*)alloc(16 * 1024 * 2);
-  float*  qb       = (float*)alloc(16 * H * 4);
-  float*  ebuf   = (float*)alloc(1280);
-  float*  alignb = (float*)alloc(1280);
-  float*  covb   = (float*)alloc(1280);
-  uint*   sflags  = (uint*)alloc(UBLK * 16 * 4);
+  float*  XiS     = (float*)alloc((size_t)320 * 2048 * 4);
+  uint*   prog    = (uint*)alloc(UBLK * 16 * 4);
   uint*   vbflags = (uint*)alloc(NV * 16 * 4);
-  uint*   vflag   = (uint*)alloc(256);
 
   float* loss = (float*)d_out;
   hipMemsetAsync(loss, 0, 4, stream);
-  hipMemsetAsync(covb, 0, 1280, stream);
-  hipMemsetAsync(h0, 0, 320 * H * 2, stream);
-  hipMemsetAsync(sh0, 0, 16 * H * 2, stream);
-  hipMemsetAsync(sflags, 0, UBLK * 16 * 4, stream);
+  hipMemsetAsync(prog, 0, UBLK * 16 * 4, stream);
   hipMemsetAsync(vbflags, 0, NV * 16 * 4, stream);
-  hipMemsetAsync(vflag, 0, 256, stream);
 
   {
     PrepP P = {articles, summaries, emb_src, emb_tgt,
@@ -829,11 +825,8 @@
     P.wdWh = wdWh; P.sdWi = sdWi; P.sdWh = sdWh; P.attnWh = attnWh; P.Wout = Wout;
     P.se_b = se_b; P.b_feat = b_feat; P.sd_b = sd_b; P.b_out = b_out;
     P.attn_wc = attn_wc; P.attn_v = attn_v; P.articles = articles;
-    P.h0 = h0; P.h1 = h1; P.XiS = XiS; P.sh0 = sh0; P.sh1 = sh1;
-    P.sent_out = sent_out; P.sent_out_bf = sent_out_bf; P.sent_feat = sent_feat;
-    P.wh_bf = wh_bf; P.sdh_bf = sdh_bf; P.final_bf = final_bf; P.catb = catb;
-    P.qb = qb; P.ebuf = ebuf; P.alignb = alignb; P.covb = covb; P.loss = loss;
-    P.sflags = sflags; P.vbflags = vbflags; P.vflag = vflag;
+    P.XiS = XiS; P.wh_bf = wh_bf; P.loss = loss;
+    P.prog = prog; P.vbflags = vbflags;
     P.Wv = W_vocab; P.Wv_bf = Wv_bf; P.bv = b_vocab; P.partials = partials;
     mega_kernel<<<MEGA, 512, 0, stream>>>(P);
   }
```

New measurement: 11.44 ms. +127.4%, slower.
